# Kernel tuning notes

Measured on AMD Instinct MI355X. Metric: run time of the kernel, lower is better.

## Reference

```python
import jax, jax.numpy as jnp
import numpy as np

NH, NKV, HD = 16, 8, 128  # heads, kv heads, head dim
N_REP = NH // NKV
EPS = 1e-06
K_MASK = float(jnp.finfo(jnp.bfloat16).min)
SCALE = HD ** -0.5


def _rms_norm(x, w):
    xf = x.astype(jnp.float32)
    rms = jnp.sqrt(jnp.mean(xf * xf, axis=-1, keepdims=True) + EPS)
    return (xf / rms * w).astype(x.dtype)


def _rotate_half(x):
    x1, x2 = jnp.split(x, 2, axis=-1)
    return jnp.concatenate([-x2, x1], axis=-1)


def setup_inputs() -> dict:
    key = jax.random.key(0)
    ks = jax.random.split(key, 5)
    B, S, H = 1, 2048, 2048
    hidden_states = jax.random.normal(ks[0], (B, S, H), jnp.float32)
    # real RoPE tables (duplicated-half layout), theta = 5e6
    pos = jnp.arange(S, dtype=jnp.float32)
    inv_freq = 1.0 / (5_000_000.0 ** (jnp.arange(0, HD, 2, dtype=jnp.float32) / HD))
    ang = pos[:, None] * inv_freq[None, :]            # (S, HD/2)
    emb = jnp.concatenate([ang, ang], axis=-1)[None]  # (1, S, HD)
    cos, sin = jnp.cos(emb), jnp.sin(emb)
    attention_mask = jnp.tril(jnp.ones((S, S), bool))[None, None]  # causal (1,1,S,S)
    sc = 0.02
    wq = jax.random.normal(ks[1], (H, NH * HD), jnp.float32) * sc
    wk = jax.random.normal(ks[2], (H, NKV * HD), jnp.float32) * sc
    wv = jax.random.normal(ks[3], (H, NKV * HD), jnp.float32) * sc
    wo = jax.random.normal(ks[4], (NH * HD, H), jnp.float32) * sc
    q_norm_w = jnp.ones((HD,), jnp.float32)
    k_norm_w = jnp.ones((HD,), jnp.float32)
    return {"hidden_states": hidden_states, "cos": cos, "sin": sin,
            "attention_mask": attention_mask, "wq": wq, "wk": wk, "wv": wv,
            "wo": wo, "q_norm_w": q_norm_w, "k_norm_w": k_norm_w}


def reference(hidden_states, cos, sin, attention_mask, wq, wk, wv, wo, q_norm_w, k_norm_w):
    B, S, H = hidden_states.shape
    q = (hidden_states @ wq).reshape(B, S, NH, HD)
    k = (hidden_states @ wk).reshape(B, S, NKV, HD)
    v = (hidden_states @ wv).reshape(B, S, NKV, HD)
    q = _rms_norm(q, q_norm_w)
    k = _rms_norm(k, k_norm_w)
    c = cos[:, :, None, :]
    s = sin[:, :, None, :]
    q = q * c + _rotate_half(q) * s
    k = k * c + _rotate_half(k) * s
    # GQA: group q heads by kv head; same math as jnp.repeat + matmul
    qg = q.reshape(B, S, NKV, N_REP, HD)
    scores = jnp.einsum('bqgrd,bkgd->bgrqk', qg, k) * SCALE  # (B,NKV,N_REP,S,S)
    scores = jnp.where(attention_mask[:, :, None], scores, K_MASK)
    attn = jax.nn.softmax(scores.astype(jnp.float32), axis=-1).astype(q.dtype)
    out = jnp.einsum('bgrqk,bkgd->bqgrd', attn, v)            # (B,S,NKV,N_REP,HD)
    out = out.reshape(B, S, NH * HD)
    return out @ wo
```

## Files before the change

### kernel.cpp

```cpp
#include <hip/hip_runtime.h>
#include <hip/hip_bf16.h>
#include <stdint.h>

typedef _Float16 half8 __attribute__((ext_vector_type(8)));
typedef _Float16 half4 __attribute__((ext_vector_type(4)));
typedef float f32x4 __attribute__((ext_vector_type(4)));

#define MFMA16(A, B, C) __builtin_amdgcn_mfma_f32_16x16x32_f16(A, B, C, 0, 0, 0)

static constexpr int Sdim = 2048;
static constexpr int NH = 16;
static constexpr int NKV = 8;
static constexpr int HD = 128;
static constexpr float ATT_SCALE = 0.08838834764831845f;
static constexpr float S0 = 4.0f;

__device__ __forceinline__ void async_copy16(const _Float16* g, _Float16* l) {
  auto gp = reinterpret_cast<const __attribute__((address_space(1))) uint32_t*>(
      reinterpret_cast<uintptr_t>(g));
  auto lp = reinterpret_cast<__attribute__((address_space(3))) uint32_t*>(
      reinterpret_cast<uintptr_t>(l));
  __builtin_amdgcn_global_load_lds(gp, lp, 16, 0, 0);
}

__global__ __launch_bounds__(256) void xconv(const float* __restrict__ X,
                                             _Float16* __restrict__ Xh) {
  int i = (blockIdx.x * 256 + threadIdx.x) * 4;
  float4 v = *(const float4*)(X + i);
  half4 h = {(_Float16)v.x, (_Float16)v.y, (_Float16)v.z, (_Float16)v.w};
  *(half4*)(Xh + i) = h;
}

__global__ __launch_bounds__(256) void wtrans_all(const float* __restrict__ wq,
                                                  const float* __restrict__ wk,
                                                  const float* __restrict__ wv,
                                                  const float* __restrict__ wo,
                                                  _Float16* __restrict__ wqT,
                                                  _Float16* __restrict__ wkT,
                                                  _Float16* __restrict__ wvT,
                                                  _Float16* __restrict__ woT) {
  const float* W;
  _Float16* WT;
  int N;
  switch (blockIdx.z) {
    case 0: W = wq; WT = wqT; N = 2048; break;
    case 1: W = wk; WT = wkT; N = 1024; break;
    case 2: W = wv; WT = wvT; N = 1024; break;
    default: W = wo; WT = woT; N = 2048; break;
  }
  if ((int)blockIdx.x * 64 >= N) return;
  const int K = 2048;
  __shared__ __align__(16) float tile[64][68];
  int n0 = blockIdx.x * 64, k0 = blockIdx.y * 64;
  int t = threadIdx.x;
  int c = (t & 15) * 4;
  int rb = t >> 4;
  for (int p = 0; p < 4; ++p) {
    int k = p * 16 + rb;
    *(float4*)&tile[k][c] = *(const float4*)(W + (size_t)(k0 + k) * N + n0 + c);
  }
  __syncthreads();
  int n = t >> 2;
  int kc = (t & 3) * 16;
  half8 o0, o1;
  for (int i = 0; i < 8; ++i) {
    o0[i] = (_Float16)tile[kc + i][n];
    o1[i] = (_Float16)tile[kc + 8 + i][n];
  }
  _Float16* dst = WT + (size_t)(n0 + n) * K + k0 + kc;
  *(half8*)dst = o0;
  *(half8*)(dst + 8) = o1;
}

template <int NI>
__device__ __forceinline__ void stage64(const _Float16* __restrict__ src, size_t stride,
                                        int k0, _Float16* lds, int w, int lane) {
  for (int ii = 0; ii < NI; ++ii) {
    int i = w * NI + ii;
    int row = i * 8 + (lane >> 3);
    int c = (lane & 7) ^ (row & 7);
    async_copy16(src + (size_t)row * stride + k0 + c * 8, lds + i * 512);
  }
}

__device__ __forceinline__ int frag_off(int row, int ks, int quad, int col) {
  return row * 64 + (((ks << 2) | quad) ^ (col & 7)) * 8;
}

__global__ __launch_bounds__(256) void gemm_qkv(const _Float16* __restrict__ Xh,
                                                const _Float16* __restrict__ wqT,
                                                const _Float16* __restrict__ wkT,
                                                const _Float16* __restrict__ wvT,
                                                _Float16* __restrict__ Q,
                                                _Float16* __restrict__ K,
                                                _Float16* __restrict__ Vt) {
  __shared__ __align__(16) _Float16 As[128 * 64];
  __shared__ __align__(16) _Float16 Bs[128 * 64];
  int bx = blockIdx.x, m0 = blockIdx.y * 128;
  const _Float16* BT;
  _Float16* outp;
  int n0, Nst;
  bool vt;
  if (bx < 16)      { BT = wqT; outp = Q;  n0 = bx * 128;        vt = false; Nst = 2048; }
  else if (bx < 24) { BT = wkT; outp = K;  n0 = (bx - 16) * 128; vt = false; Nst = 1024; }
  else              { BT = wvT; outp = Vt; n0 = (bx - 24) * 128; vt = true;  Nst = 2048; }
  int t = threadIdx.x, lane = t & 63, w = t >> 6;
  int col = lane & 15, quad = lane >> 4;
  int wm = (w & 1) * 64, wn = (w >> 1) * 64;
  f32x4 acc[4][4] = {};
  for (int k0 = 0; k0 < 2048; k0 += 64) {
    stage64<4>(Xh + (size_t)m0 * 2048, 2048, k0, As, w, lane);
    stage64<4>(BT + (size_t)n0 * 2048, 2048, k0, Bs, w, lane);
    __syncthreads();
    half8 af[4][2], bf[4][2];
    for (int i = 0; i < 4; ++i)
      for (int ks = 0; ks < 2; ++ks) {
        af[i][ks] = *(const half8*)(As + frag_off(wm + i * 16 + col, ks, quad, col));
        bf[i][ks] = *(const half8*)(Bs + frag_off(wn + i * 16 + col, ks, quad, col));
      }
    if (!vt) {
      for (int ks = 0; ks < 2; ++ks)
        for (int i = 0; i < 4; ++i)
          for (int j = 0; j < 4; ++j)
            acc[i][j] = MFMA16(bf[j][ks], af[i][ks], acc[i][j]);
    } else {
      for (int ks = 0; ks < 2; ++ks)
        for (int i = 0; i < 4; ++i)
          for (int j = 0; j < 4; ++j)
            acc[i][j] = MFMA16(af[i][ks], bf[j][ks], acc[i][j]);
    }
    __syncthreads();
  }
  if (!vt) {
    for (int i = 0; i < 4; ++i)
      for (int j = 0; j < 4; ++j) {
        int m = m0 + wm + i * 16 + col;
        int n = n0 + wn + j * 16 + quad * 4;
        half4 hv = {(_Float16)acc[i][j][0], (_Float16)acc[i][j][1],
                    (_Float16)acc[i][j][2], (_Float16)acc[i][j][3]};
        *(half4*)(outp + (size_t)m * Nst + n) = hv;
      }
  } else {
    for (int i = 0; i < 4; ++i)
      for (int j = 0; j < 4; ++j) {
        int n = n0 + wn + j * 16 + col;
        int mb = m0 + wm + i * 16 + quad * 4;
        half4 hv = {(_Float16)acc[i][j][0], (_Float16)acc[i][j][1],
                    (_Float16)acc[i][j][2], (_Float16)acc[i][j][3]};
        *(half4*)(outp + (size_t)n * Sdim + mb) = hv;
      }
  }
}

__global__ __launch_bounds__(256) void gemm_o(const _Float16* __restrict__ A,
                                              const _Float16* __restrict__ BT,
                                              float* __restrict__ C) {
  __shared__ __align__(16) _Float16 As[64 * 64];
  __shared__ __align__(16) _Float16 Bs[128 * 64];
  int m0 = blockIdx.y * 64, n0 = blockIdx.x * 128;
  int t = threadIdx.x, lane = t & 63, w = t >> 6;
  int col = lane & 15, quad = lane >> 4;
  int wm = (w & 1) * 32, wn = (w >> 1) * 64;
  f32x4 acc[2][4] = {};
  for (int k0 = 0; k0 < 2048; k0 += 64) {
    stage64<2>(A + (size_t)m0 * 2048, 2048, k0, As, w, lane);
    stage64<4>(BT + (size_t)n0 * 2048, 2048, k0, Bs, w, lane);
    __syncthreads();
    half8 af[2][2], bf[4][2];
    for (int ks = 0; ks < 2; ++ks) {
      for (int i = 0; i < 2; ++i)
        af[i][ks] = *(const half8*)(As + frag_off(wm + i * 16 + col, ks, quad, col));
      for (int j = 0; j < 4; ++j)
        bf[j][ks] = *(const half8*)(Bs + frag_off(wn + j * 16 + col, ks, quad, col));
    }
    for (int ks = 0; ks < 2; ++ks)
      for (int i = 0; i < 2; ++i)
        for (int j = 0; j < 4; ++j)
          acc[i][j] = MFMA16(bf[j][ks], af[i][ks], acc[i][j]);
    __syncthreads();
  }
  for (int i = 0; i < 2; ++i)
    for (int j = 0; j < 4; ++j) {
      int m = m0 + wm + i * 16 + col;
      int n = n0 + wn + j * 16 + quad * 4;
      *(f32x4*)(C + (size_t)m * 2048 + n) = acc[i][j];
    }
}

__global__ __launch_bounds__(256) void rmsrope_all(const _Float16* __restrict__ Qraw,
                                                   const _Float16* __restrict__ Kraw,
                                                   _Float16* __restrict__ Qn,
                                                   _Float16* __restrict__ Kn,
                                                   const float* __restrict__ cs,
                                                   const float* __restrict__ sn,
                                                   const float* __restrict__ qw,
                                                   const float* __restrict__ kw) {
  int w = threadIdx.x >> 6, lane = threadIdx.x & 63;
  int gw = blockIdx.x * 4 + w;
  const _Float16* src;
  _Float16* dst;
  const float* nw;
  int m, h, nh;
  float scale;
  if (gw < Sdim * NH) {
    m = gw >> 4; h = gw & 15; nh = NH; src = Qraw; dst = Qn; nw = qw; scale = ATT_SCALE;
  } else {
    int g2 = gw - Sdim * NH;
    m = g2 >> 3; h = g2 & 7; nh = NKV; src = Kraw; dst = Kn; nw = kw; scale = 1.0f;
  }
  const _Float16* p = src + (size_t)m * nh * HD + h * HD;
  float x0 = (float)p[lane], x1 = (float)p[lane + 64];
  float ss = x0 * x0 + x1 * x1;
#pragma unroll
  for (int o = 32; o > 0; o >>= 1) ss += __shfl_xor(ss, o);
  float inv = rsqrtf(ss * (1.0f / 128.0f) + 1e-6f);
  float n0v = x0 * inv * nw[lane], n1v = x1 * inv * nw[lane + 64];
  float c0 = cs[m * HD + lane], c1 = cs[m * HD + lane + 64];
  float s0 = sn[m * HD + lane], s1 = sn[m * HD + lane + 64];
  _Float16* q = dst + (size_t)m * nh * HD + h * HD;
  q[lane] = (_Float16)((n0v * c0 - n1v * s0) * scale);
  q[lane + 64] = (_Float16)((n1v * c1 + n0v * s1) * scale);
}

__global__ __launch_bounds__(256) void fattn(const _Float16* __restrict__ Qn,
                                             const _Float16* __restrict__ Kn,
                                             const _Float16* __restrict__ Vt,
                                             _Float16* __restrict__ Op01,
                                             _Float16* __restrict__ Op2,
                                             float* __restrict__ lp) {
  __shared__ __align__(16) _Float16 Ks[64 * 128];
  __shared__ __align__(16) _Float16 Vs[128 * 64];
  __shared__ __align__(16) _Float16 Ps[4 * 1024];
  int xb = blockIdx.x;
  int h = blockIdx.y, g = h >> 1, s = blockIdx.z;
  int t = threadIdx.x, lane = t & 63, w = t >> 6;
  int col = lane & 15, quad = lane >> 4;
  _Float16* Psw = Ps + w * 1024;
  _Float16* op = (s == 2) ? Op2 : Op01 + (size_t)s * Sdim * (NH * HD);
  float* lpp = lp + (size_t)s * NH * Sdim + (size_t)h * Sdim;
#pragma unroll 1
  for (int tile = 0; tile < 2; ++tile) {
    int qb = tile ? xb : 31 - xb;
    half8 qf[4];
    {
      int qrow = qb * 64 + w * 16 + col;
      for (int kc = 0; kc < 4; ++kc)
        qf[kc] = *(const half8*)(Qn + (size_t)qrow * (NH * HD) + h * HD + kc * 32 + quad * 8);
    }
    f32x4 O[8] = {};
    float li[4] = {0.0f, 0.0f, 0.0f, 0.0f};
    for (int kt = s; kt <= qb; kt += 3) {
      for (int ii = 0; ii < 4; ++ii) {
        int i = w * 4 + ii;
        int krow = i * 4 + (lane >> 4);
        int kc = (lane & 15) ^ (krow & 15);
        async_copy16(Kn + (size_t)(kt * 64 + krow) * (NKV * HD) + g * HD + kc * 8,
                     Ks + i * 512);
        int vrow = i * 8 + (lane >> 3);
        int vc = (lane & 7) ^ (vrow & 7);
        async_copy16(Vt + (size_t)(g * HD + vrow) * Sdim + kt * 64 + vc * 8,
                     Vs + i * 512);
      }
      __syncthreads();
      f32x4 Sc[4];
      for (int nt = 0; nt < 4; ++nt) {
        f32x4 a = {};
        for (int kc = 0; kc < 4; ++kc) {
          half8 b = *(const half8*)(Ks + (nt * 16 + col) * 128 + ((4 * kc + quad) ^ col) * 8);
          a = MFMA16(qf[kc], b, a);
        }
        Sc[nt] = a;
      }
      if (kt == qb) {
        for (int nt = 0; nt < 4; ++nt)
          for (int r = 0; r < 4; ++r)
            if ((nt * 16 + col) > (w * 16 + quad * 4 + r)) Sc[nt][r] = -1e4f;
      }
      for (int nt = 0; nt < 4; ++nt)
        for (int r = 0; r < 4; ++r) {
          float pv = __expf(Sc[nt][r] - S0);
          Sc[nt][r] = pv;
          li[r] += pv;
        }
      for (int nt = 0; nt < 4; ++nt)
        for (int r = 0; r < 4; ++r) {
          int q = quad * 4 + r;
          Psw[q * 64 + (((2 * nt + (col >> 3)) ^ (q & 7)) * 8) + (col & 7)] =
              (_Float16)Sc[nt][r];
        }
      for (int c2 = 0; c2 < 2; ++c2) {
        half8 ap = *(const half8*)(Psw + col * 64 + (((4 * c2 + quad) ^ (col & 7)) * 8));
        for (int nt = 0; nt < 8; ++nt) {
          half8 bv = *(const half8*)(Vs + (nt * 16 + col) * 64 +
                                     (((4 * c2 + quad) ^ (col & 7)) * 8));
          O[nt] = MFMA16(ap, bv, O[nt]);
        }
      }
      __syncthreads();
    }
    for (int r = 0; r < 4; ++r) {
      float sm = li[r];
      sm += __shfl_xor(sm, 1);
      sm += __shfl_xor(sm, 2);
      sm += __shfl_xor(sm, 4);
      sm += __shfl_xor(sm, 8);
      li[r] = sm;
    }
    for (int nt = 0; nt < 8; ++nt)
      for (int r = 0; r < 4; ++r) {
        int m = qb * 64 + w * 16 + quad * 4 + r;
        op[(size_t)m * (NH * HD) + h * HD + nt * 16 + col] = (_Float16)O[nt][r];
      }
    if (col == 0) {
      for (int r = 0; r < 4; ++r) lpp[qb * 64 + w * 16 + quad * 4 + r] = li[r];
    }
  }
}

__global__ __launch_bounds__(256) void merge(const _Float16* __restrict__ Op01,
                                             const _Float16* __restrict__ Op2,
                                             const float* __restrict__ lp,
                                             _Float16* __restrict__ attn) {
  int m = blockIdx.x, t = threadIdx.x;
  int h = t >> 4, d0 = (t & 15) * 8;
  size_t off = (size_t)m * (NH * HD) + h * HD + d0;
  half8 o0 = *(const half8*)(Op01 + off);
  half8 o1 = *(const half8*)(Op01 + (size_t)Sdim * NH * HD + off);
  half8 o2 = *(const half8*)(Op2 + off);
  float l = lp[(size_t)h * Sdim + m] +
            lp[(size_t)NH * Sdim + (size_t)h * Sdim + m] +
            lp[2 * (size_t)NH * Sdim + (size_t)h * Sdim + m];
  float ri = 1.0f / l;
  half8 o;
  for (int i = 0; i < 8; ++i)
    o[i] = (_Float16)(((float)o0[i] + (float)o1[i] + (float)o2[i]) * ri);
  *(half8*)(attn + off) = o;
}

extern "C" void kernel_launch(void* const* d_in, const int* in_sizes, int n_in,
                              void* d_out, int out_size, void* d_ws, size_t ws_size,
                              hipStream_t stream) {
  (void)in_sizes; (void)n_in; (void)out_size; (void)ws_size;
  const float* X  = (const float*)d_in[0];
  const float* cs = (const float*)d_in[1];
  const float* sn = (const float*)d_in[2];
  const float* wq = (const float*)d_in[4];
  const float* wk = (const float*)d_in[5];
  const float* wv = (const float*)d_in[6];
  const float* wo = (const float*)d_in[7];
  const float* qw = (const float*)d_in[8];
  const float* kw = (const float*)d_in[9];
  char* ws = (char*)d_ws;
  const size_t MB = 1024 * 1024;
  _Float16* wqT  = (_Float16*)(ws + 0 * MB);
  _Float16* wkT  = (_Float16*)(ws + 8 * MB);
  _Float16* wvT  = (_Float16*)(ws + 12 * MB);
  _Float16* woT  = (_Float16*)(ws + 16 * MB);
  _Float16* Xh   = (_Float16*)(ws + 24 * MB);
  _Float16* Qraw = (_Float16*)(ws + 32 * MB);
  _Float16* Kraw = (_Float16*)(ws + 40 * MB);
  _Float16* Vt   = (_Float16*)(ws + 44 * MB);
  _Float16* Qn   = (_Float16*)(ws + 48 * MB);
  _Float16* Kn   = (_Float16*)(ws + 56 * MB);
  float*    lp   = (float*)(ws + 60 * MB);
  _Float16* Op01 = wqT;
  _Float16* Op2  = Xh;
  _Float16* attn = Qraw;
  float* out = (float*)d_out;

  xconv<<<4096, 256, 0, stream>>>(X, Xh);
  wtrans_all<<<dim3(32, 32, 4), 256, 0, stream>>>(wq, wk, wv, wo, wqT, wkT, wvT, woT);

  gemm_qkv<<<dim3(32, 16), 256, 0, stream>>>(Xh, wqT, wkT, wvT, Qraw, Kraw, Vt);

  rmsrope_all<<<(Sdim * NH + Sdim * NKV) / 4, 256, 0, stream>>>(Qraw, Kraw, Qn, Kn,
                                                                cs, sn, qw, kw);

  fattn<<<dim3(16, 16, 3), 256, 0, stream>>>(Qn, Kn, Vt, Op01, Op2, lp);
  merge<<<2048, 256, 0, stream>>>(Op01, Op2, lp, attn);

  gemm_o<<<dim3(16, 32), 256, 0, stream>>>(attn, woT, out);
}
```

Baseline: 270.5 us.

## Double-buffer KV tiles, share them across paired query tiles, split KV two ways

The attention kernel now processes both paired query tiles (31-xb and xb) in one pass over the KV range, so each K/V tile is loaded once and reused for both instead of being reloaded per tile. K/V staging is double-buffered so the next tile's async loads overlap compute on the current one. The KV split goes from three ways to two, which removes the third partial output and simplifies the merge. Blocks are remapped with a swizzled 1D grid. The cost is more shared memory and registers (two accumulator sets), which may lower occupancy, and half as many blocks.

```diff
diff --git a/kernel.cpp b/kernel.cpp
--- a/kernel.cpp
+++ b/kernel.cpp
@@ -222,82 +222,110 @@
   q[lane + 64] = (_Float16)((n1v * c1 + n0v * s1) * scale);
 }
 
+__device__ __forceinline__ void attn_tile(const half8* qf, f32x4* O, float* li,
+                                          const _Float16* Ksb, const _Float16* Vsb,
+                                          _Float16* Psw, bool domask,
+                                          int col, int quad, int w) {
+  f32x4 Sc[4];
+  for (int nt = 0; nt < 4; ++nt) {
+    f32x4 a = {};
+    for (int kc = 0; kc < 4; ++kc) {
+      half8 b = *(const half8*)(Ksb + (nt * 16 + col) * 128 + ((4 * kc + quad) ^ col) * 8);
+      a = MFMA16(qf[kc], b, a);
+    }
+    Sc[nt] = a;
+  }
+  if (domask) {
+    for (int nt = 0; nt < 4; ++nt)
+      for (int r = 0; r < 4; ++r)
+        if ((nt * 16 + col) > (w * 16 + quad * 4 + r)) Sc[nt][r] = -1e4f;
+  }
+  for (int nt = 0; nt < 4; ++nt)
+    for (int r = 0; r < 4; ++r) {
+      float pv = __expf(Sc[nt][r] - S0);
+      Sc[nt][r] = pv;
+      li[r] += pv;
+    }
+  for (int nt = 0; nt < 4; ++nt)
+    for (int r = 0; r < 4; ++r) {
+      int q = quad * 4 + r;
+      Psw[q * 64 + (((2 * nt + (col >> 3)) ^ (q & 7)) * 8) + (col & 7)] =
+          (_Float16)Sc[nt][r];
+    }
+  for (int c2 = 0; c2 < 2; ++c2) {
+    half8 ap = *(const half8*)(Psw + col * 64 + (((4 * c2 + quad) ^ (col & 7)) * 8));
+    for (int nt = 0; nt < 8; ++nt) {
+      half8 bv = *(const half8*)(Vsb + (nt * 16 + col) * 64 +
+                                 (((4 * c2 + quad) ^ (col & 7)) * 8));
+      O[nt] = MFMA16(ap, bv, O[nt]);
+    }
+  }
+}
+
 __global__ __launch_bounds__(256) void fattn(const _Float16* __restrict__ Qn,
                                              const _Float16* __restrict__ Kn,
                                              const _Float16* __restrict__ Vt,
                                              _Float16* __restrict__ Op01,
-                                             _Float16* __restrict__ Op2,
                                              float* __restrict__ lp) {
-  __shared__ __align__(16) _Float16 Ks[64 * 128];
-  __shared__ __align__(16) _Float16 Vs[128 * 64];
+  __shared__ __align__(16) _Float16 Ks[2][64 * 128];
+  __shared__ __align__(16) _Float16 Vs[2][128 * 64];
   __shared__ __align__(16) _Float16 Ps[4 * 1024];
-  int xb = blockIdx.x;
-  int h = blockIdx.y, g = h >> 1, s = blockIdx.z;
+  int f = blockIdx.x;
+  int Wk = (f & 7) * 64 + (f >> 3);
+  int xb = Wk & 15, h = (Wk >> 4) & 15, s = Wk >> 8;
+  int g = h >> 1;
+  int qb0 = 31 - xb, qb1 = xb;
   int t = threadIdx.x, lane = t & 63, w = t >> 6;
   int col = lane & 15, quad = lane >> 4;
   _Float16* Psw = Ps + w * 1024;
-  _Float16* op = (s == 2) ? Op2 : Op01 + (size_t)s * Sdim * (NH * HD);
+  _Float16* op = Op01 + (size_t)s * Sdim * (NH * HD);
   float* lpp = lp + (size_t)s * NH * Sdim + (size_t)h * Sdim;
+
+  auto stageKV = [&](int b, int kt) {
+    for (int ii = 0; ii < 4; ++ii) {
+      int i = w * 4 + ii;
+      int krow = i * 4 + (lane >> 4);
+      int kc = (lane & 15) ^ (krow & 15);
+      async_copy16(Kn + (size_t)(kt * 64 + krow) * (NKV * HD) + g * HD + kc * 8,
+                   Ks[b] + i * 512);
+      int vrow = i * 8 + (lane >> 3);
+      int vc = (lane & 7) ^ (vrow & 7);
+      async_copy16(Vt + (size_t)(g * HD + vrow) * Sdim + kt * 64 + vc * 8,
+                   Vs[b] + i * 512);
+    }
+  };
+
+  half8 qf0[4], qf1[4];
+  {
+    int qr0 = qb0 * 64 + w * 16 + col;
+    int qr1 = qb1 * 64 + w * 16 + col;
+    for (int kc = 0; kc < 4; ++kc) {
+      qf0[kc] = *(const half8*)(Qn + (size_t)qr0 * (NH * HD) + h * HD + kc * 32 + quad * 8);
+      qf1[kc] = *(const half8*)(Qn + (size_t)qr1 * (NH * HD) + h * HD + kc * 32 + quad * 8);
+    }
+  }
+  f32x4 O0[8] = {}, O1[8] = {};
+  float li0[4] = {}, li1[4] = {};
+
+  int nt = (qb0 - s) / 2 + 1;
+  stageKV(0, s);
+  __syncthreads();
 #pragma unroll 1
-  for (int tile = 0; tile < 2; ++tile) {
-    int qb = tile ? xb : 31 - xb;
-    half8 qf[4];
-    {
-      int qrow = qb * 64 + w * 16 + col;
-      for (int kc = 0; kc < 4; ++kc)
-        qf[kc] = *(const half8*)(Qn + (size_t)qrow * (NH * HD) + h * HD + kc * 32 + quad * 8);
-    }
-    f32x4 O[8] = {};
-    float li[4] = {0.0f, 0.0f, 0.0f, 0.0f};
-    for (int kt = s; kt <= qb; kt += 3) {
-      for (int ii = 0; ii < 4; ++ii) {
-        int i = w * 4 + ii;
-        int krow = i * 4 + (lane >> 4);
-        int kc = (lane & 15) ^ (krow & 15);
-        async_copy16(Kn + (size_t)(kt * 64 + krow) * (NKV * HD) + g * HD + kc * 8,
-                     Ks + i * 512);
-        int vrow = i * 8 + (lane >> 3);
-        int vc = (lane & 7) ^ (vrow & 7);
-        async_copy16(Vt + (size_t)(g * HD + vrow) * Sdim + kt * 64 + vc * 8,
-                     Vs + i * 512);
-      }
-      __syncthreads();
-      f32x4 Sc[4];
-      for (int nt = 0; nt < 4; ++nt) {
-        f32x4 a = {};
-        for (int kc = 0; kc < 4; ++kc) {
-          half8 b = *(const half8*)(Ks + (nt * 16 + col) * 128 + ((4 * kc + quad) ^ col) * 8);
-          a = MFMA16(qf[kc], b, a);
-        }
-        Sc[nt] = a;
-      }
-      if (kt == qb) {
-        for (int nt = 0; nt < 4; ++nt)
-          for (int r = 0; r < 4; ++r)
-            if ((nt * 16 + col) > (w * 16 + quad * 4 + r)) Sc[nt][r] = -1e4f;
-      }
-      for (int nt = 0; nt < 4; ++nt)
-        for (int r = 0; r < 4; ++r) {
-          float pv = __expf(Sc[nt][r] - S0);
-          Sc[nt][r] = pv;
-          li[r] += pv;
-        }
-      for (int nt = 0; nt < 4; ++nt)
-        for (int r = 0; r < 4; ++r) {
-          int q = quad * 4 + r;
-          Psw[q * 64 + (((2 * nt + (col >> 3)) ^ (q & 7)) * 8) + (col & 7)] =
-              (_Float16)Sc[nt][r];
-        }
-      for (int c2 = 0; c2 < 2; ++c2) {
-        half8 ap = *(const half8*)(Psw + col * 64 + (((4 * c2 + quad) ^ (col & 7)) * 8));
-        for (int nt = 0; nt < 8; ++nt) {
-          half8 bv = *(const half8*)(Vs + (nt * 16 + col) * 64 +
-                                     (((4 * c2 + quad) ^ (col & 7)) * 8));
-          O[nt] = MFMA16(ap, bv, O[nt]);
-        }
-      }
-      __syncthreads();
-    }
+  for (int it = 0; it < nt; ++it) {
+    int kt = s + it * 2;
+    if (it + 1 < nt) stageKV((it + 1) & 1, kt + 2);
+    const _Float16* Kb = Ks[it & 1];
+    const _Float16* Vb = Vs[it & 1];
+    if (kt <= qb1) {
+      attn_tile(qf0, O0, li0, Kb, Vb, Psw, false, col, quad, w);
+      attn_tile(qf1, O1, li1, Kb, Vb, Psw, kt == qb1, col, quad, w);
+    } else {
+      attn_tile(qf0, O0, li0, Kb, Vb, Psw, kt == qb0, col, quad, w);
+    }
+    __syncthreads();
+  }
+
+  auto finish = [&](f32x4* O, float* li, int qb) {
     for (int r = 0; r < 4; ++r) {
       float sm = li[r];
       sm += __shfl_xor(sm, 1);
@@ -306,19 +334,19 @@
       sm += __shfl_xor(sm, 8);
       li[r] = sm;
     }
-    for (int nt = 0; nt < 8; ++nt)
+    for (int ntile = 0; ntile < 8; ++ntile)
       for (int r = 0; r < 4; ++r) {
         int m = qb * 64 + w * 16 + quad * 4 + r;
-        op[(size_t)m * (NH * HD) + h * HD + nt * 16 + col] = (_Float16)O[nt][r];
+        op[(size_t)m * (NH * HD) + h * HD + ntile * 16 + col] = (_Float16)O[ntile][r];
       }
-    if (col == 0) {
+    if (col == 0)
       for (int r = 0; r < 4; ++r) lpp[qb * 64 + w * 16 + quad * 4 + r] = li[r];
-    }
-  }
+  };
+  finish(O0, li0, qb0);
+  finish(O1, li1, qb1);
 }
 
 __global__ __launch_bounds__(256) void merge(const _Float16* __restrict__ Op01,
-                                             const _Float16* __restrict__ Op2,
                                              const float* __restrict__ lp,
                                              _Float16* __restrict__ attn) {
   int m = blockIdx.x, t = threadIdx.x;
@@ -326,14 +354,12 @@
   size_t off = (size_t)m * (NH * HD) + h * HD + d0;
   half8 o0 = *(const half8*)(Op01 + off);
   half8 o1 = *(const half8*)(Op01 + (size_t)Sdim * NH * HD + off);
-  half8 o2 = *(const half8*)(Op2 + off);
   float l = lp[(size_t)h * Sdim + m] +
-            lp[(size_t)NH * Sdim + (size_t)h * Sdim + m] +
-            lp[2 * (size_t)NH * Sdim + (size_t)h * Sdim + m];
+            lp[(size_t)NH * Sdim + (size_t)h * Sdim + m];
   float ri = 1.0f / l;
   half8 o;
   for (int i = 0; i < 8; ++i)
-    o[i] = (_Float16)(((float)o0[i] + (float)o1[i] + (float)o2[i]) * ri);
+    o[i] = (_Float16)(((float)o0[i] + (float)o1[i]) * ri);
   *(half8*)(attn + off) = o;
 }
 
@@ -364,7 +390,6 @@
   _Float16* Kn   = (_Float16*)(ws + 56 * MB);
   float*    lp   = (float*)(ws + 60 * MB);
   _Float16* Op01 = wqT;
-  _Float16* Op2  = Xh;
   _Float16* attn = Qraw;
   float* out = (float*)d_out;
 
@@ -376,8 +401,8 @@
   rmsrope_all<<<(Sdim * NH + Sdim * NKV) / 4, 256, 0, stream>>>(Qraw, Kraw, Qn, Kn,
                                                                 cs, sn, qw, kw);
 
-  fattn<<<dim3(16, 16, 3), 256, 0, stream>>>(Qn, Kn, Vt, Op01, Op2, lp);
-  merge<<<2048, 256, 0, stream>>>(Op01, Op2, lp, attn);
+  fattn<<<512, 256, 0, stream>>>(Qn, Kn, Vt, Op01, lp);
+  merge<<<2048, 256, 0, stream>>>(Op01, lp, attn);
 
   gemm_o<<<dim3(16, 32), 256, 0, stream>>>(attn, woT, out);
 }
```

Result: no change. 275.1 us (+1.7%).
